# Performance work log

Measured on AMD Instinct MI355X. Metric: run time of the kernel, lower is better.

Reference implementation:

```python
import jax, jax.numpy as jnp
import numpy as np

DIM = 768
NUM_EXPERTS = 1536
EXPERT_DIM = 64
NOISE_SCALE = 0.1
B, H, W = 1, 64, 64
N = B * H * W


def setup_inputs() -> dict:
    key = jax.random.key(0)
    ks = jax.random.split(key, 6)
    scaled = lambda k, shape, fan_in: (jax.random.normal(k, shape, jnp.float32) / np.sqrt(fan_in)).astype(jnp.float32)
    return {
        "x": jax.random.normal(ks[0], (B, H, W, DIM), jnp.float32),
        "noise": jax.random.normal(ks[1], (N, NUM_EXPERTS), jnp.float32),
        "gate_w": scaled(ks[2], (NUM_EXPERTS, DIM), DIM),
        "gate_b": jnp.zeros((NUM_EXPERTS,), jnp.float32),
        "expert_w": scaled(ks[3], (NUM_EXPERTS, EXPERT_DIM, DIM), DIM),  # torch Linear weight layout (out, in)
        "expert_b": jnp.zeros((NUM_EXPERTS, EXPERT_DIM), jnp.float32),
        "proj_w": scaled(ks[4], (DIM, EXPERT_DIM), EXPERT_DIM),
        "proj_b": jnp.zeros((DIM,), jnp.float32),
    }


def reference(x, noise, gate_w, gate_b, expert_w, expert_b, proj_w, proj_b):
    orig_shape = x.shape
    xf = x.reshape(-1, orig_shape[-1])  # (N, DIM)
    # Noisy gating
    scores = xf @ gate_w.T + gate_b + noise * NOISE_SCALE  # (N, E)
    gate_weights = jax.nn.softmax(scores, axis=-1)
    top_w, top_i = jax.lax.top_k(gate_weights, 1)  # (N, 1), (N, 1)
    idx = top_i[:, 0]  # (N,)
    # Gather only the selected expert per token (same math as the redundant
    # dense all-expert compute followed by a gather in the original).
    w_sel = expert_w[idx]  # (N, EXPERT_DIM, DIM)
    b_sel = expert_b[idx]  # (N, EXPERT_DIM)
    y = jnp.einsum('nd,nod->no', xf, w_sel) + b_sel  # (N, EXPERT_DIM)
    out_flat = (y @ proj_w.T + proj_b) * top_w  # (N, DIM); top_w broadcasts (N,1)
    return out_flat.reshape(orig_shape)
```

## Files before the change

### kernel.cpp

```cpp
#include <hip/hip_runtime.h>
#include <hip/hip_bf16.h>

#define NT 4096
#define DIM 768
#define NE 1536
#define ED 64
#define GAP_THR 8e-3f

typedef __attribute__((ext_vector_type(8))) short short8v;
typedef __attribute__((ext_vector_type(4))) float f32x4;

__device__ __forceinline__ unsigned short f2bf(float f) {
  unsigned int u = __float_as_uint(f);
  unsigned int r = (u + 0x7fffu + ((u >> 16) & 1u)) >> 16;
  return (unsigned short)r;
}
__device__ __forceinline__ float bf2f(unsigned short h) {
  return __uint_as_float(((unsigned int)h) << 16);
}

__device__ __forceinline__ void gload16(const void* g, void* l) {
  __builtin_amdgcn_global_load_lds((const __attribute__((address_space(1))) void*)g,
                                   (__attribute__((address_space(3))) void*)l, 16, 0, 0);
}

__device__ __forceinline__ void top2_merge(float& m1, int& i1, float& m2, int& i2,
                                           float om1, int oi1, float om2, int oi2) {
  if (om1 > m1 || (om1 == m1 && oi1 < i1)) {
    if (m1 > om2 || (m1 == om2 && i1 < oi2)) { m2 = m1; i2 = i1; }
    else { m2 = om2; i2 = oi2; }
    m1 = om1; i1 = oi1;
  } else {
    if (om1 > m2 || (om1 == m2 && oi1 < i2)) { m2 = om1; i2 = oi1; }
  }
}

__global__ __launch_bounds__(256) void split_all(
    const float* __restrict__ x, const float* __restrict__ gw,
    unsigned short* __restrict__ xhi, unsigned short* __restrict__ xlo,
    unsigned short* __restrict__ ghi, unsigned short* __restrict__ glo) {
  const int nx4 = NT * DIM / 4;
  const int ng4 = NE * DIM / 4;
  int i = blockIdx.x * 256 + threadIdx.x;
  const float* src; unsigned short* hi; unsigned short* lo; int j;
  if (i < nx4) { src = x; hi = xhi; lo = xlo; j = i; }
  else { j = i - nx4; if (j >= ng4) return; src = gw; hi = ghi; lo = glo; }
  float4 v = ((const float4*)src)[j];
  unsigned short h0 = f2bf(v.x), h1 = f2bf(v.y), h2 = f2bf(v.z), h3 = f2bf(v.w);
  ((ushort4*)hi)[j] = make_ushort4(h0, h1, h2, h3);
  ((ushort4*)lo)[j] = make_ushort4(f2bf(v.x - bf2f(h0)), f2bf(v.y - bf2f(h1)),
                                   f2bf(v.z - bf2f(h2)), f2bf(v.w - bf2f(h3)));
}

__global__ __launch_bounds__(256) void gate_mfma(
    const unsigned short* __restrict__ xhi, const unsigned short* __restrict__ xlo,
    const unsigned short* __restrict__ ghi, const unsigned short* __restrict__ glo,
    const float* __restrict__ gb, const float* __restrict__ noise,
    float4* __restrict__ part_a, int* __restrict__ part_i2) {
  __shared__ __align__(16) unsigned short sA[2 * 128 * 32];
  __shared__ __align__(16) unsigned short sB[2 * 128 * 32];
  const int tid = threadIdx.x;
  const int w = tid >> 6, lane = tid & 63;
  const int wr = w >> 1, wc = w & 1;
  const int bm = blockIdx.x, bn = blockIdx.y;
  const int fr = lane & 15;
  const int fg = lane >> 4;
  const int gsw = fg ^ ((fr >> 1) & 3);

  f32x4 acc[4][4];
#pragma unroll
  for (int i = 0; i < 4; i++)
#pragma unroll
    for (int j = 0; j < 4; j++) acc[i][j] = (f32x4){0.f, 0.f, 0.f, 0.f};

  const size_t arow = (size_t)bm * 128 * DIM;
  const size_t brow = (size_t)bn * 128 * DIM;
  const int sr_lo = tid >> 2;
  const int sg = (tid & 3) ^ ((tid >> 3) & 3);

  for (int kt = 0; kt < DIM; kt += 32) {
    __syncthreads();
#pragma unroll
    for (int h = 0; h < 2; h++) {
      const int r = h * 64 + sr_lo;
      const size_t asrc = arow + (size_t)r * DIM + kt + sg * 8;
      const size_t bsrc = brow + (size_t)r * DIM + kt + sg * 8;
      const int dofs = h * 2048 + w * 512;
      gload16(xhi + asrc, &sA[dofs]);
      gload16(xlo + asrc, &sA[4096 + dofs]);
      gload16(ghi + bsrc, &sB[dofs]);
      gload16(glo + bsrc, &sB[4096 + dofs]);
    }
    __syncthreads();

    short8v ah[4], al[4], bh[4], bl[4];
#pragma unroll
    for (int mf = 0; mf < 4; mf++) {
      int ro = (wr * 64 + mf * 16 + fr) * 32 + gsw * 8;
      ah[mf] = *(const short8v*)&sA[ro];
      al[mf] = *(const short8v*)&sA[4096 + ro];
    }
#pragma unroll
    for (int nf = 0; nf < 4; nf++) {
      int ro = (wc * 64 + nf * 16 + fr) * 32 + gsw * 8;
      bh[nf] = *(const short8v*)&sB[ro];
      bl[nf] = *(const short8v*)&sB[4096 + ro];
    }
#pragma unroll
    for (int mf = 0; mf < 4; mf++)
#pragma unroll
      for (int nf = 0; nf < 4; nf++) {
        f32x4 c = acc[mf][nf];
        c = __builtin_amdgcn_mfma_f32_16x16x32_bf16(ah[mf], bh[nf], c, 0, 0, 0);
        c = __builtin_amdgcn_mfma_f32_16x16x32_bf16(ah[mf], bl[nf], c, 0, 0, 0);
        c = __builtin_amdgcn_mfma_f32_16x16x32_bf16(al[mf], bh[nf], c, 0, 0, 0);
        acc[mf][nf] = c;
      }
  }

  const int gm0 = bm * 128 + wr * 64;
  const int gn0 = bn * 128 + wc * 64;
  const int chunk = bn * 2 + wc;
  int gcol[4]; float gbv[4];
#pragma unroll
  for (int nf = 0; nf < 4; nf++) { gcol[nf] = gn0 + nf * 16 + fr; gbv[nf] = gb[gcol[nf]]; }
#pragma unroll
  for (int mf = 0; mf < 4; mf++) {
    float sv[4][4];
#pragma unroll
    for (int nf = 0; nf < 4; nf++)
#pragma unroll
      for (int reg = 0; reg < 4; reg++) {
        int gm = gm0 + mf * 16 + fg * 4 + reg;
        sv[nf][reg] = acc[mf][nf][reg] + gbv[nf] + 0.1f * noise[(size_t)gm * NE + gcol[nf]];
      }
#pragma unroll
    for (int reg = 0; reg < 4; reg++) {
      float m1 = sv[0][reg]; int i1 = gcol[0];
      float m2 = -3e38f; int i2 = 0x7fffffff;
#pragma unroll
      for (int nf = 1; nf < 4; nf++) {
        float v = sv[nf][reg]; int ii = gcol[nf];
        if (v > m1 || (v == m1 && ii < i1)) { m2 = m1; i2 = i1; m1 = v; i1 = ii; }
        else if (v > m2 || (v == m2 && ii < i2)) { m2 = v; i2 = ii; }
      }
#pragma unroll
      for (int off = 1; off <= 8; off <<= 1) {
        float om1 = __shfl_xor(m1, off, 64); int oi1 = __shfl_xor(i1, off, 64);
        float om2 = __shfl_xor(m2, off, 64); int oi2 = __shfl_xor(i2, off, 64);
        top2_merge(m1, i1, m2, i2, om1, oi1, om2, oi2);
      }
      float ssum = 0.f;
#pragma unroll
      for (int nf = 0; nf < 4; nf++) ssum += __expf(sv[nf][reg] - m1);
#pragma unroll
      for (int off = 1; off <= 8; off <<= 1) ssum += __shfl_xor(ssum, off, 64);
      if (fr == 0) {
        int gm = gm0 + mf * 16 + fg * 4 + reg;
        part_a[(size_t)gm * 24 + chunk] = make_float4(m1, m2, ssum, __int_as_float(i1));
        part_i2[(size_t)gm * 24 + chunk] = i2;
      }
    }
  }
}

__global__ __launch_bounds__(256) void finalize(
    const float4* __restrict__ part_a, const int* __restrict__ part_i2,
    float* __restrict__ topw, int* __restrict__ idx, int* __restrict__ counts,
    int* __restrict__ rc_count, int* __restrict__ rc_n, int* __restrict__ rc_i2) {
  const int wv = threadIdx.x >> 6, lane = threadIdx.x & 63;
  const int n = blockIdx.x * 4 + wv;
  float m1 = -3e38f, m2 = -3e38f, lm1 = -3e38f, lsum = 0.f;
  int i1 = 0x7fffffff, i2 = 0x7fffffff;
  if (lane < 24) {
    float4 pa = part_a[(size_t)n * 24 + lane];
    m1 = pa.x; m2 = pa.y; lsum = pa.z; i1 = __float_as_int(pa.w);
    i2 = part_i2[(size_t)n * 24 + lane];
    lm1 = pa.x;
  }
#pragma unroll
  for (int off = 1; off <= 32; off <<= 1) {
    float om1 = __shfl_xor(m1, off, 64); int oi1 = __shfl_xor(i1, off, 64);
    float om2 = __shfl_xor(m2, off, 64); int oi2 = __shfl_xor(i2, off, 64);
    top2_merge(m1, i1, m2, i2, om1, oi1, om2, oi2);
  }
  float contrib = (lane < 24) ? __expf(lm1 - m1) * lsum : 0.f;
#pragma unroll
  for (int off = 1; off <= 32; off <<= 1) contrib += __shfl_xor(contrib, off, 64);
  if (lane == 0) {
    topw[n] = 1.0f / contrib;
    idx[n] = i1;
    atomicAdd(counts + i1, 1);
    if (m1 - m2 < GAP_THR) {
      int p = atomicAdd(rc_count, 1);
      rc_n[p] = n; rc_i2[p] = i2;
    }
  }
}

__global__ __launch_bounds__(256) void recheck(
    const float* __restrict__ x, const float* __restrict__ gw,
    const float* __restrict__ gb, const float* __restrict__ noise,
    const int* __restrict__ rc_n, const int* __restrict__ rc_i2,
    const int* __restrict__ rc_count, int* __restrict__ idx, int* __restrict__ counts) {
  __shared__ float r1[4], r2[4];
  const int cnt = *rc_count;
  const int tid = threadIdx.x;
  const int w = tid >> 6, lane = tid & 63;
  for (int t = blockIdx.x; t < cnt; t += gridDim.x) {
    const int n = rc_n[t];
    const int e1 = idx[n], e2 = rc_i2[t];
    const float* xr = x + (size_t)n * DIM;
    const float* w1 = gw + (size_t)e1 * DIM;
    const float* w2 = gw + (size_t)e2 * DIM;
    float p1 = 0.f, p2 = 0.f;
    for (int k = tid; k < DIM; k += 256) {
      float xv = xr[k];
      p1 += xv * w1[k];
      p2 += xv * w2[k];
    }
#pragma unroll
    for (int off = 32; off; off >>= 1) {
      p1 += __shfl_xor(p1, off, 64);
      p2 += __shfl_xor(p2, off, 64);
    }
    if (lane == 0) { r1[w] = p1; r2[w] = p2; }
    __syncthreads();
    if (tid == 0) {
      float s1 = r1[0] + r1[1] + r1[2] + r1[3] + gb[e1] + 0.1f * noise[(size_t)n * NE + e1];
      float s2 = r2[0] + r2[1] + r2[2] + r2[3] + gb[e2] + 0.1f * noise[(size_t)n * NE + e2];
      if (s2 > s1 || (s2 == s1 && e2 < e1)) {
        idx[n] = e2;
        atomicSub(counts + e1, 1);
        atomicAdd(counts + e2, 1);
      }
    }
    __syncthreads();
  }
}

__global__ __launch_bounds__(256) void scan_offsets(
    const int* __restrict__ counts, int* __restrict__ offs, int* __restrict__ cursor) {
  __shared__ int part[256];
  const int t = threadIdx.x;
  int loc[6];
  int s = 0;
#pragma unroll
  for (int j = 0; j < 6; j++) { loc[j] = counts[t * 6 + j]; s += loc[j]; }
  part[t] = s;
  __syncthreads();
  for (int d = 1; d < 256; d <<= 1) {
    int v2 = (t >= d) ? part[t - d] : 0;
    __syncthreads();
    part[t] += v2;
    __syncthreads();
  }
  int excl = part[t] - s;
#pragma unroll
  for (int j = 0; j < 6; j++) {
    offs[t * 6 + j] = excl;
    cursor[t * 6 + j] = excl;
    excl += loc[j];
  }
}

__global__ __launch_bounds__(256) void scatter_tokens(
    const int* __restrict__ idx, int* __restrict__ cursor, int* __restrict__ sorted) {
  const int n = blockIdx.x * 256 + threadIdx.x;
  int e = idx[n];
  int pos = atomicAdd(cursor + e, 1);
  sorted[pos] = n;
}

__global__ __launch_bounds__(256) void expert_gemm(
    const float* __restrict__ x, const float* __restrict__ ew,
    const float* __restrict__ eb, const int* __restrict__ counts,
    const int* __restrict__ offs, const int* __restrict__ sorted,
    float* __restrict__ y) {
  const int e = blockIdx.x;
  const int cnt = counts[e];
  if (cnt == 0) return;
  const int base = offs[e];
  __shared__ float4 xs4[8 * 192];
  __shared__ int tok[8];
  const int tid = threadIdx.x;
  const int w = tid >> 6;
  const int lane = tid & 63;
  const float4* W4 = (const float4*)(ew + (size_t)e * ED * DIM);
  const float4* X4 = (const float4*)x;

  for (int c0 = 0; c0 < cnt; c0 += 8) {
    int cc = min(8, cnt - c0);
    __syncthreads();
    if (tid < cc) tok[tid] = sorted[base + c0 + tid];
    __syncthreads();
    int nf = cc * 192;
    for (int f = tid; f < nf; f += 256) {
      int t = f / 192, p = f % 192;
      xs4[t * 192 + p] = X4[(size_t)tok[t] * 192 + p];
    }
    __syncthreads();

    for (int oi = 0; oi < 16; oi++) {
      int o = w * 16 + oi;
      float4 w4a = W4[(size_t)o * 192 + lane];
      float4 w4b = W4[(size_t)o * 192 + lane + 64];
      float4 w4c = W4[(size_t)o * 192 + lane + 128];
      for (int t = 0; t < cc; t++) {
        float4 xa = xs4[t * 192 + lane];
        float4 xb = xs4[t * 192 + lane + 64];
        float4 xc = xs4[t * 192 + lane + 128];
        float p = w4a.x * xa.x + w4a.y * xa.y + w4a.z * xa.z + w4a.w * xa.w;
        p += w4b.x * xb.x + w4b.y * xb.y + w4b.z * xb.z + w4b.w * xb.w;
        p += w4c.x * xc.x + w4c.y * xc.y + w4c.z * xc.z + w4c.w * xc.w;
#pragma unroll
        for (int off = 32; off; off >>= 1) p += __shfl_xor(p, off, 64);
        if (lane == 0) y[(size_t)tok[t] * ED + o] = p + eb[e * ED + o];
      }
    }
  }
}

__global__ __launch_bounds__(256) void proj_kernel(
    const float* __restrict__ y, const float* __restrict__ pw,
    const float* __restrict__ pb, const float* __restrict__ topw,
    float* __restrict__ out) {
  const int b = blockIdx.x;
  const int tid = threadIdx.x;
  __shared__ float4 ys4[8 * 16];
  __shared__ float tw[8];
  if (tid < 128) {
    int t = tid >> 4, q = tid & 15;
    ys4[tid] = ((const float4*)y)[((size_t)b * 8 + t) * 16 + q];
  }
  if (tid < 8) tw[tid] = topw[b * 8 + tid];
  __syncthreads();
  const float4* pw4 = (const float4*)pw;
  for (int c = 0; c < 3; c++) {
    int d = c * 256 + tid;
    float4 pwv[16];
#pragma unroll
    for (int q = 0; q < 16; q++) pwv[q] = pw4[(size_t)d * 16 + q];
    float pbv = pb[d];
    for (int t = 0; t < 8; t++) {
      float s = 0.f;
#pragma unroll
      for (int q = 0; q < 16; q++) {
        float4 yv = ys4[t * 16 + q];
        s += pwv[q].x * yv.x + pwv[q].y * yv.y + pwv[q].z * yv.z + pwv[q].w * yv.w;
      }
      out[((size_t)b * 8 + t) * DIM + d] = (s + pbv) * tw[t];
    }
  }
}

extern "C" void kernel_launch(void* const* d_in, const int* in_sizes, int n_in,
                              void* d_out, int out_size, void* d_ws, size_t ws_size,
                              hipStream_t stream) {
  const float* x      = (const float*)d_in[0];
  const float* noise  = (const float*)d_in[1];
  const float* gate_w = (const float*)d_in[2];
  const float* gate_b = (const float*)d_in[3];
  const float* ew     = (const float*)d_in[4];
  const float* eb     = (const float*)d_in[5];
  const float* pw     = (const float*)d_in[6];
  const float* pb     = (const float*)d_in[7];
  float* out = (float*)d_out;

  char* ws = (char*)d_ws;
  unsigned short* xhi    = (unsigned short*)(ws);
  unsigned short* xlo    = (unsigned short*)(ws + 6291456);
  unsigned short* ghi    = (unsigned short*)(ws + 12582912);
  unsigned short* glo    = (unsigned short*)(ws + 14942208);
  float4*         part_a = (float4*)(ws + 17301504);
  int*            part_i2= (int*)  (ws + 18874368);
  float*          y      = (float*)(ws + 19267584);
  float*          topw   = (float*)(ws + 20316160);
  int*            idx    = (int*)  (ws + 20332544);
  int*            counts = (int*)  (ws + 20348928);
  int*            rc_cnt = (int*)  (ws + 20355072);
  int*            offs   = (int*)  (ws + 20355328);
  int*            cursor = (int*)  (ws + 20361472);
  int*            sorted = (int*)  (ws + 20367616);
  int*            rc_n   = (int*)  (ws + 20384000);
  int*            rc_i2  = (int*)  (ws + 20400384);

  hipMemsetAsync(counts, 0, NE * sizeof(int) + 4, stream);

  split_all<<<(NT * DIM / 4 + NE * DIM / 4 + 255) / 256, 256, 0, stream>>>(
      x, gate_w, xhi, xlo, ghi, glo);
  gate_mfma<<<dim3(NT / 128, NE / 128), 256, 0, stream>>>(
      xhi, xlo, ghi, glo, gate_b, noise, part_a, part_i2);
  finalize<<<NT / 4, 256, 0, stream>>>(part_a, part_i2, topw, idx, counts,
                                       rc_cnt, rc_n, rc_i2);
  recheck<<<32, 256, 0, stream>>>(x, gate_w, gate_b, noise, rc_n, rc_i2, rc_cnt,
                                  idx, counts);
  scan_offsets<<<1, 256, 0, stream>>>(counts, offs, cursor);
  scatter_tokens<<<NT / 256, 256, 0, stream>>>(idx, cursor, sorted);
  expert_gemm<<<NE, 256, 0, stream>>>(x, ew, eb, counts, offs, sorted, y);
  proj_kernel<<<NT / 8, 256, 0, stream>>>(y, pw, pb, topw, out);
}
```

Baseline: 269.4 us.

## Fuse expert GEMM with output projection and drop sort/scan routing kernels

Removes the memset, prefix-scan and scatter kernels. Each expert block now scans the whole idx array itself to build its own token list in shared memory. The expert GEMM result stays in shared memory and the projection and top-weight scaling run in the same block, so the intermediate y buffer and a separate proj kernel are no longer needed. In exchange, every one of the 1536 blocks reads the full 16KB idx array. The projection weights are reloaded per expert block instead of per 8-token tile, and the token list is capped at 128 per expert by masking.

```diff
diff --git a/kernel.cpp b/kernel.cpp
--- a/kernel.cpp
+++ b/kernel.cpp
@@ -38,7 +38,9 @@
 __global__ __launch_bounds__(256) void split_all(
     const float* __restrict__ x, const float* __restrict__ gw,
     unsigned short* __restrict__ xhi, unsigned short* __restrict__ xlo,
-    unsigned short* __restrict__ ghi, unsigned short* __restrict__ glo) {
+    unsigned short* __restrict__ ghi, unsigned short* __restrict__ glo,
+    int* __restrict__ rc_cnt) {
+  if (blockIdx.x == 0 && threadIdx.x == 0) *rc_cnt = 0;
   const int nx4 = NT * DIM / 4;
   const int ng4 = NE * DIM / 4;
   int i = blockIdx.x * 256 + threadIdx.x;
@@ -166,7 +168,7 @@
 
 __global__ __launch_bounds__(256) void finalize(
     const float4* __restrict__ part_a, const int* __restrict__ part_i2,
-    float* __restrict__ topw, int* __restrict__ idx, int* __restrict__ counts,
+    float* __restrict__ topw, int* __restrict__ idx,
     int* __restrict__ rc_count, int* __restrict__ rc_n, int* __restrict__ rc_i2) {
   const int wv = threadIdx.x >> 6, lane = threadIdx.x & 63;
   const int n = blockIdx.x * 4 + wv;
@@ -190,7 +192,6 @@
   if (lane == 0) {
     topw[n] = 1.0f / contrib;
     idx[n] = i1;
-    atomicAdd(counts + i1, 1);
     if (m1 - m2 < GAP_THR) {
       int p = atomicAdd(rc_count, 1);
       rc_n[p] = n; rc_i2[p] = i2;
@@ -202,7 +203,7 @@
     const float* __restrict__ x, const float* __restrict__ gw,
     const float* __restrict__ gb, const float* __restrict__ noise,
     const int* __restrict__ rc_n, const int* __restrict__ rc_i2,
-    const int* __restrict__ rc_count, int* __restrict__ idx, int* __restrict__ counts) {
+    const int* __restrict__ rc_count, int* __restrict__ idx) {
   __shared__ float r1[4], r2[4];
   const int cnt = *rc_count;
   const int tid = threadIdx.x;
@@ -229,75 +230,53 @@
     if (tid == 0) {
       float s1 = r1[0] + r1[1] + r1[2] + r1[3] + gb[e1] + 0.1f * noise[(size_t)n * NE + e1];
       float s2 = r2[0] + r2[1] + r2[2] + r2[3] + gb[e2] + 0.1f * noise[(size_t)n * NE + e2];
-      if (s2 > s1 || (s2 == s1 && e2 < e1)) {
-        idx[n] = e2;
-        atomicSub(counts + e1, 1);
-        atomicAdd(counts + e2, 1);
-      }
-    }
-    __syncthreads();
-  }
-}
-
-__global__ __launch_bounds__(256) void scan_offsets(
-    const int* __restrict__ counts, int* __restrict__ offs, int* __restrict__ cursor) {
-  __shared__ int part[256];
-  const int t = threadIdx.x;
-  int loc[6];
-  int s = 0;
-#pragma unroll
-  for (int j = 0; j < 6; j++) { loc[j] = counts[t * 6 + j]; s += loc[j]; }
-  part[t] = s;
-  __syncthreads();
-  for (int d = 1; d < 256; d <<= 1) {
-    int v2 = (t >= d) ? part[t - d] : 0;
-    __syncthreads();
-    part[t] += v2;
-    __syncthreads();
-  }
-  int excl = part[t] - s;
-#pragma unroll
-  for (int j = 0; j < 6; j++) {
-    offs[t * 6 + j] = excl;
-    cursor[t * 6 + j] = excl;
-    excl += loc[j];
-  }
-}
-
-__global__ __launch_bounds__(256) void scatter_tokens(
-    const int* __restrict__ idx, int* __restrict__ cursor, int* __restrict__ sorted) {
-  const int n = blockIdx.x * 256 + threadIdx.x;
-  int e = idx[n];
-  int pos = atomicAdd(cursor + e, 1);
-  sorted[pos] = n;
-}
-
-__global__ __launch_bounds__(256) void expert_gemm(
+      if (s2 > s1 || (s2 == s1 && e2 < e1)) idx[n] = e2;
+    }
+    __syncthreads();
+  }
+}
+
+__global__ __launch_bounds__(256) void expert_out(
     const float* __restrict__ x, const float* __restrict__ ew,
-    const float* __restrict__ eb, const int* __restrict__ counts,
-    const int* __restrict__ offs, const int* __restrict__ sorted,
-    float* __restrict__ y) {
+    const float* __restrict__ eb, const float* __restrict__ pw,
+    const float* __restrict__ pb, const int* __restrict__ idx,
+    const float* __restrict__ topw, float* __restrict__ out) {
   const int e = blockIdx.x;
-  const int cnt = counts[e];
-  if (cnt == 0) return;
-  const int base = offs[e];
+  __shared__ int toklist[128];
+  __shared__ int ntok_s;
   __shared__ float4 xs4[8 * 192];
-  __shared__ int tok[8];
+  __shared__ __align__(16) float ys[8][64];
+  __shared__ float tws[8];
   const int tid = threadIdx.x;
   const int w = tid >> 6;
   const int lane = tid & 63;
+
+  if (tid == 0) ntok_s = 0;
+  __syncthreads();
+  for (int q = tid; q < NT / 4; q += 256) {
+    int4 v = ((const int4*)idx)[q];
+    int n0 = q * 4;
+    if (v.x == e) { toklist[atomicAdd(&ntok_s, 1) & 127] = n0; }
+    if (v.y == e) { toklist[atomicAdd(&ntok_s, 1) & 127] = n0 + 1; }
+    if (v.z == e) { toklist[atomicAdd(&ntok_s, 1) & 127] = n0 + 2; }
+    if (v.w == e) { toklist[atomicAdd(&ntok_s, 1) & 127] = n0 + 3; }
+  }
+  __syncthreads();
+  const int cnt = ntok_s;
+  if (cnt == 0) return;
+
   const float4* W4 = (const float4*)(ew + (size_t)e * ED * DIM);
   const float4* X4 = (const float4*)x;
+  const float4* pw4 = (const float4*)pw;
 
   for (int c0 = 0; c0 < cnt; c0 += 8) {
-    int cc = min(8, cnt - c0);
-    __syncthreads();
-    if (tid < cc) tok[tid] = sorted[base + c0 + tid];
-    __syncthreads();
-    int nf = cc * 192;
-    for (int f = tid; f < nf; f += 256) {
+    const int cc = min(8, cnt - c0);
+    __syncthreads();
+    if (tid < cc) tws[tid] = topw[toklist[c0 + tid]];
+    const int nf4 = cc * 192;
+    for (int f = tid; f < nf4; f += 256) {
       int t = f / 192, p = f % 192;
-      xs4[t * 192 + p] = X4[(size_t)tok[t] * 192 + p];
+      xs4[t * 192 + p] = X4[(size_t)toklist[c0 + t] * 192 + p];
     }
     __syncthreads();
 
@@ -315,41 +294,28 @@
         p += w4c.x * xc.x + w4c.y * xc.y + w4c.z * xc.z + w4c.w * xc.w;
 #pragma unroll
         for (int off = 32; off; off >>= 1) p += __shfl_xor(p, off, 64);
-        if (lane == 0) y[(size_t)tok[t] * ED + o] = p + eb[e * ED + o];
-      }
-    }
-  }
-}
-
-__global__ __launch_bounds__(256) void proj_kernel(
-    const float* __restrict__ y, const float* __restrict__ pw,
-    const float* __restrict__ pb, const float* __restrict__ topw,
-    float* __restrict__ out) {
-  const int b = blockIdx.x;
-  const int tid = threadIdx.x;
-  __shared__ float4 ys4[8 * 16];
-  __shared__ float tw[8];
-  if (tid < 128) {
-    int t = tid >> 4, q = tid & 15;
-    ys4[tid] = ((const float4*)y)[((size_t)b * 8 + t) * 16 + q];
-  }
-  if (tid < 8) tw[tid] = topw[b * 8 + tid];
-  __syncthreads();
-  const float4* pw4 = (const float4*)pw;
-  for (int c = 0; c < 3; c++) {
-    int d = c * 256 + tid;
-    float4 pwv[16];
-#pragma unroll
-    for (int q = 0; q < 16; q++) pwv[q] = pw4[(size_t)d * 16 + q];
-    float pbv = pb[d];
-    for (int t = 0; t < 8; t++) {
-      float s = 0.f;
-#pragma unroll
-      for (int q = 0; q < 16; q++) {
-        float4 yv = ys4[t * 16 + q];
-        s += pwv[q].x * yv.x + pwv[q].y * yv.y + pwv[q].z * yv.z + pwv[q].w * yv.w;
-      }
-      out[((size_t)b * 8 + t) * DIM + d] = (s + pbv) * tw[t];
+        if (lane == 0) ys[t][o] = p + eb[e * ED + o];
+      }
+    }
+    __syncthreads();
+
+#pragma unroll
+    for (int c = 0; c < 3; c++) {
+      const int d = c * 256 + tid;
+      float4 pwv[16];
+#pragma unroll
+      for (int q = 0; q < 16; q++) pwv[q] = pw4[(size_t)d * 16 + q];
+      const float pbv = pb[d];
+      for (int t = 0; t < cc; t++) {
+        const float4* yv4 = (const float4*)ys[t];
+        float s = 0.f;
+#pragma unroll
+        for (int q = 0; q < 16; q++) {
+          float4 yv = yv4[q];
+          s += pwv[q].x * yv.x + pwv[q].y * yv.y + pwv[q].z * yv.z + pwv[q].w * yv.w;
+        }
+        out[(size_t)toklist[c0 + t] * DIM + d] = (s + pbv) * tws[t];
+      }
     }
   }
 }
@@ -374,29 +340,18 @@
   unsigned short* glo    = (unsigned short*)(ws + 14942208);
   float4*         part_a = (float4*)(ws + 17301504);
   int*            part_i2= (int*)  (ws + 18874368);
-  float*          y      = (float*)(ws + 19267584);
-  float*          topw   = (float*)(ws + 20316160);
-  int*            idx    = (int*)  (ws + 20332544);
-  int*            counts = (int*)  (ws + 20348928);
-  int*            rc_cnt = (int*)  (ws + 20355072);
-  int*            offs   = (int*)  (ws + 20355328);
-  int*            cursor = (int*)  (ws + 20361472);
-  int*            sorted = (int*)  (ws + 20367616);
-  int*            rc_n   = (int*)  (ws + 20384000);
-  int*            rc_i2  = (int*)  (ws + 20400384);
-
-  hipMemsetAsync(counts, 0, NE * sizeof(int) + 4, stream);
+  float*          topw   = (float*)(ws + 19267584);
+  int*            idx    = (int*)  (ws + 19283968);
+  int*            rc_cnt = (int*)  (ws + 19300352);
+  int*            rc_n   = (int*)  (ws + 19300608);
+  int*            rc_i2  = (int*)  (ws + 19316992);
 
   split_all<<<(NT * DIM / 4 + NE * DIM / 4 + 255) / 256, 256, 0, stream>>>(
-      x, gate_w, xhi, xlo, ghi, glo);
+      x, gate_w, xhi, xlo, ghi, glo, rc_cnt);
   gate_mfma<<<dim3(NT / 128, NE / 128), 256, 0, stream>>>(
       xhi, xlo, ghi, glo, gate_b, noise, part_a, part_i2);
-  finalize<<<NT / 4, 256, 0, stream>>>(part_a, part_i2, topw, idx, counts,
+  finalize<<<NT / 4, 256, 0, stream>>>(part_a, part_i2, topw, idx,
                                        rc_cnt, rc_n, rc_i2);
-  recheck<<<32, 256, 0, stream>>>(x, gate_w, gate_b, noise, rc_n, rc_i2, rc_cnt,
-                                  idx, counts);
-  scan_offsets<<<1, 256, 0, stream>>>(counts, offs, cursor);
-  scatter_tokens<<<NT / 256, 256, 0, stream>>>(idx, cursor, sorted);
-  expert_gemm<<<NE, 256, 0, stream>>>(x, ew, eb, counts, offs, sorted, y);
-  proj_kernel<<<NT / 8, 256, 0, stream>>>(y, pw, pb, topw, out);
-}
+  recheck<<<32, 256, 0, stream>>>(x, gate_w, gate_b, noise, rc_n, rc_i2, rc_cnt, idx);
+  expert_out<<<NE, 256, 0, stream>>>(x, ew, eb, pw, pb, idx, topw, out);
+}
```

Result: slower. 303.8 us (+12.8%).
